# Kernel optimization log

Measured on AMD Instinct MI355X. Metric: run time of the kernel, lower is better.

Reference implementation:

```python
import jax, jax.numpy as jnp
import numpy as np

B = 8192      # graphs per batch
NPG = 40      # nodes per graph (= average_nodes, uniform here)
DEG = 16      # avg degree
IN = 64
HID = 32
OUT = 10
K1 = 20       # ceil(0.5*40)
K2 = 10       # ceil(0.5*20)
N = B * NPG
E = N * DEG
EPS = 1e-15


def _lin_params(k, fi, fo):
    kw, kb = jax.random.split(k)
    s = 1.0 / np.sqrt(fi)
    w = jax.random.uniform(kw, (fi, fo), jnp.float32, -s, s)
    b = jax.random.uniform(kb, (fo,), jnp.float32, -s, s)
    return w, b


def setup_inputs():
    key = jax.random.key(0)
    ks = jax.random.split(key, 14)
    x = jax.random.normal(ks[0], (N, IN), jnp.float32)
    # edges constrained within each graph (graphs are contiguous blocks of NPG nodes)
    g = jnp.repeat(jnp.arange(B, dtype=jnp.int32), NPG * DEG)
    src = g * NPG + jax.random.randint(ks[1], (E,), 0, NPG, dtype=jnp.int32)
    dst = g * NPG + jax.random.randint(ks[2], (E,), 0, NPG, dtype=jnp.int32)
    edge_index = jnp.stack([src, dst])
    batch = jnp.repeat(jnp.arange(B, dtype=jnp.int32), NPG)
    w_c1, b_c1 = _lin_params(ks[3], IN, HID)
    w_p1, b_p1 = _lin_params(ks[4], HID, K1)
    w2r, b2 = _lin_params(ks[5], HID, HID)
    w2o, _ = _lin_params(ks[6], HID, HID)
    w_p2, b_p2 = _lin_params(ks[7], HID, K2)
    w3r, b3 = _lin_params(ks[8], HID, HID)
    w3o, _ = _lin_params(ks[9], HID, HID)
    w_l1, b_l1 = _lin_params(ks[10], HID, HID)
    w_l2, b_l2 = _lin_params(ks[11], HID, OUT)
    return dict(x=x, edge_index=edge_index, batch=batch,
                w_c1=w_c1, b_c1=b_c1, w_p1=w_p1, b_p1=b_p1,
                w2r=w2r, b2=b2, w2o=w2o, w_p2=w_p2, b_p2=b_p2,
                w3r=w3r, b3=b3, w3o=w3o,
                w_l1=w_l1, b_l1=b_l1, w_l2=w_l2, b_l2=b_l2)


def _gcn_conv(x, edge_index, w, b):
    # PyG GCNConv: x' = D^-1/2 (A + I) D^-1/2 (X W) + b, unit edge weights
    h = x @ w
    row, col = edge_index
    deg = jnp.zeros((N,), h.dtype).at[col].add(1.0) + 1.0  # +1 self loop
    dinv = jax.lax.rsqrt(deg)
    msg = (dinv[row] * dinv[col])[:, None] * h[row]
    out = jnp.zeros_like(h).at[col].add(msg)
    out = out + (dinv * dinv)[:, None] * h  # self-loop contribution
    return out + b


def _dense_mincut_pool(x, adj, s, mask=None):
    # faithful to torch_geometric.nn.dense_mincut_pool
    s = jax.nn.softmax(s, axis=-1)
    if mask is not None:
        m = mask[..., None].astype(x.dtype)
        x = x * m
        s = s * m
    k = s.shape[-1]
    out = jnp.einsum('bnk,bnf->bkf', s, x)
    out_adj = jnp.einsum('bnk,bnm,bml->bkl', s, adj, s)
    mincut_num = jnp.trace(out_adj, axis1=1, axis2=2)
    d_flat = adj.sum(-1)                                   # [B, n]
    mincut_den = jnp.einsum('bnk,bn,bnk->b', s, d_flat, s)  # tr(S^T D S)
    mincut_loss = jnp.mean(-(mincut_num / mincut_den))
    ss = jnp.einsum('bnk,bnl->bkl', s, s)
    ss_norm = jnp.sqrt(jnp.sum(ss * ss, axis=(1, 2), keepdims=True))
    i_s = jnp.eye(k, dtype=x.dtype) / jnp.sqrt(jnp.asarray(k, x.dtype))
    ortho_loss = jnp.mean(jnp.sqrt(jnp.sum((ss / ss_norm - i_s) ** 2, axis=(1, 2))))
    # zero diagonal, then symmetric degree-normalize coarse adjacency
    eye = jnp.eye(k, dtype=x.dtype)
    out_adj = out_adj * (1.0 - eye)
    d = jnp.sqrt(out_adj.sum(-1))[:, None, :] + EPS        # [B,1,k]
    out_adj = out_adj / d / jnp.swapaxes(d, 1, 2)
    return out, out_adj, mincut_loss, ortho_loss


def _dense_graph_conv(x, adj, w_rel, b, w_root):
    # PyG DenseGraphConv (aggr='add'): lin_rel(A @ x) + lin_root(x); lin_root bias=False
    return (adj @ x) @ w_rel + b + x @ w_root


def reference(x, edge_index, batch, w_c1, b_c1, w_p1, b_p1, w2r, b2, w2o,
              w_p2, b_p2, w3r, b3, w3o, w_l1, b_l1, w_l2, b_l2):
    h = jax.nn.relu(_gcn_conv(x, edge_index, w_c1, b_c1))
    # to_dense_batch (uniform NPG nodes per graph, batch sorted)
    local = jnp.arange(N, dtype=jnp.int32) - batch * NPG
    xd = jnp.zeros((B, NPG, HID), h.dtype).at[batch, local].set(h)
    mask = jnp.ones((B, NPG), bool)
    # to_dense_adj (accumulates duplicate edges)
    row, col = edge_index
    g = batch[row]
    adj = jnp.zeros((B, NPG, NPG), h.dtype).at[g, row - g * NPG, col - g * NPG].add(1.0)
    s = xd @ w_p1 + b_p1
    xd, adj, mc1, o1 = _dense_mincut_pool(xd, adj, s, mask)
    xd = jax.nn.relu(_dense_graph_conv(xd, adj, w2r, b2, w2o))
    s = xd @ w_p2 + b_p2
    xd, adj, mc2, o2 = _dense_mincut_pool(xd, adj, s)
    xd = _dense_graph_conv(xd, adj, w3r, b3, w3o)
    pooled = xd.mean(axis=1)
    out = jax.nn.relu(pooled @ w_l1 + b_l1) @ w_l2 + b_l2
    return out, mc1 + mc2 + o1 + o2
```

## Files before the change

### kernel.cpp

```cpp
#include <hip/hip_runtime.h>

#define NT 256

constexpr int Bg   = 8192;
constexpr int NPG  = 40;
constexpr int EPG  = 640;
constexpr int IN_  = 64;
constexpr int HID  = 32;
constexpr int K1   = 20;
constexpr int K2   = 10;
constexpr int OUTC = 10;
constexpr int NE   = Bg * NPG * 16;
constexpr int SX   = 68;
constexpr int SH   = 36;
constexpr float EPSF = 1e-15f;

#define FMA4(acc, a, b) do { \
    float _s = (a); \
    acc.x = fmaf(_s, (b).x, acc.x); \
    acc.y = fmaf(_s, (b).y, acc.y); \
    acc.z = fmaf(_s, (b).z, acc.z); \
    acc.w = fmaf(_s, (b).w, acc.w); } while (0)

__device__ __forceinline__ float wave_red(float v) {
#pragma unroll
    for (int off = 32; off > 0; off >>= 1) v += __shfl_down(v, off, 64);
    return v;
}

__global__ __launch_bounds__(NT, 4)
void mincut_fused(const float* __restrict__ x, const int* __restrict__ ei,
                  const float* __restrict__ w_c1, const float* __restrict__ b_c1,
                  const float* __restrict__ w_p1, const float* __restrict__ b_p1,
                  const float* __restrict__ w2r_, const float* __restrict__ b2_,
                  const float* __restrict__ w2o_,
                  const float* __restrict__ w_p2, const float* __restrict__ b_p2,
                  const float* __restrict__ w3r_, const float* __restrict__ b3_,
                  const float* __restrict__ w3o_,
                  const float* __restrict__ w_l1, const float* __restrict__ b_l1,
                  const float* __restrict__ w_l2, const float* __restrict__ b_l2,
                  float* __restrict__ out, float* __restrict__ wsg)
{
    __shared__ __align__(16) float sA[NPG * NPG];
    __shared__ __align__(16) float sXbuf[NPG * SX];
    __shared__ __align__(16) float sH[NPG * SH];
    __shared__ __align__(16) float sXd[NPG * SH];
    __shared__ __align__(16) float sdinv[NPG];
    __shared__ __align__(16) float srowsA[NPG];
    __shared__ __align__(16) float srowm[NPG];
    __shared__ __align__(16) float sden[NPG];
    __shared__ __align__(16) float sc[8];

    float* sA2  = sA;
    float* sS   = sXbuf;
    float* sAS  = sXbuf + 800;
    float* sSS  = sXbuf + 1600;
    float* sX2  = sH;
    float* sS2  = sH + 720;
    float* sX3  = sH + 920;
    float* sA3  = sH + 1280;
    float* sXw2o= sXd;
    float* sW3r = sXd;
    float* sW3o = sXd + 360;
    float* sX4  = sH;

    const int g    = blockIdx.x;
    const int tid  = threadIdx.x;
    const int lane = tid & 63;
    const int wid  = tid >> 6;

    int er0, ec0, er1, ec1, er2 = -1, ec2 = 0;
    {
        const int eb = g * EPG, nb = g * NPG;
        int e = eb + tid;
        er0 = ei[e] - nb; ec0 = ei[NE + e] - nb;
        e += NT;
        er1 = ei[e] - nb; ec1 = ei[NE + e] - nb;
        if (tid + 2 * NT < EPG) {
            e += NT;
            er2 = ei[e] - nb; ec2 = ei[NE + e] - nb;
        }
    }
    for (int i = tid; i < NPG * NPG; i += NT) sA[i] = 0.f;
    {
        const float4* xg = (const float4*)(x + (size_t)g * (NPG * IN_));
        for (int i = tid; i < NPG * (IN_ / 4); i += NT) {
            int n = i >> 4, k = i & 15;
            ((float4*)(sXbuf + n * SX))[k] = xg[i];
        }
    }
    __syncthreads();

    atomicAdd(&sA[er0 * NPG + ec0], 1.f);
    atomicAdd(&sA[er1 * NPG + ec1], 1.f);
    if (er2 >= 0) atomicAdd(&sA[er2 * NPG + ec2], 1.f);

    if (tid < 160) {
        int np = tid >> 3, fq = tid & 7;
        int n0 = 2 * np, n1 = n0 + 1;
        const float4* a0p = (const float4*)(sXbuf + n0 * SX);
        const float4* a1p = (const float4*)(sXbuf + n1 * SX);
        const float4* wg  = (const float4*)w_c1;
        float4 acc0 = {0.f,0.f,0.f,0.f}, acc1 = {0.f,0.f,0.f,0.f};
#pragma unroll 4
        for (int kk = 0; kk < IN_ / 4; kk++) {
            float4 a0 = a0p[kk], a1 = a1p[kk];
            float4 w0 = wg[(4*kk+0)*8 + fq];
            float4 w1 = wg[(4*kk+1)*8 + fq];
            float4 w2 = wg[(4*kk+2)*8 + fq];
            float4 w3 = wg[(4*kk+3)*8 + fq];
            FMA4(acc0, a0.x, w0); FMA4(acc0, a0.y, w1);
            FMA4(acc0, a0.z, w2); FMA4(acc0, a0.w, w3);
            FMA4(acc1, a1.x, w0); FMA4(acc1, a1.y, w1);
            FMA4(acc1, a1.z, w2); FMA4(acc1, a1.w, w3);
        }
        ((float4*)(sH + n0 * SH))[fq] = acc0;
        ((float4*)(sH + n1 * SH))[fq] = acc1;
    }
    __syncthreads();

    if (tid < NPG) {
        float s = 0.f;
#pragma unroll
        for (int r = 0; r < NPG; r++) s += sA[r * NPG + tid];
        sdinv[tid] = rsqrtf(s + 1.f);
    } else if (tid >= 64 && tid < 64 + NPG) {
        int n = tid - 64; float s = 0.f;
#pragma unroll
        for (int m = 0; m < NPG; m++) s += sA[n * NPG + m];
        srowsA[n] = s;
    }
    __syncthreads();

    if (tid < 160) {
        int cp = tid >> 3, fq = tid & 7;
        int c0 = 2 * cp, c1 = c0 + 1;
        float4 acc0 = {0.f,0.f,0.f,0.f}, acc1 = {0.f,0.f,0.f,0.f};
#pragma unroll 8
        for (int r = 0; r < NPG; r++) {
            float2 a2 = *(const float2*)&sA[r * NPG + c0];
            float dv = sdinv[r];
            float4 bv = ((const float4*)(sH + r * SH))[fq];
            FMA4(acc0, a2.x * dv, bv);
            FMA4(acc1, a2.y * dv, bv);
        }
        float4 bb = ((const float4*)b_c1)[fq];
        float4 h0 = ((const float4*)(sH + c0 * SH))[fq];
        float4 h1 = ((const float4*)(sH + c1 * SH))[fq];
        float d0 = sdinv[c0], d1 = sdinv[c1];
        float4 r0, r1;
        r0.x = fmaxf(fmaf(d0, fmaf(d0, h0.x, acc0.x), bb.x), 0.f);
        r0.y = fmaxf(fmaf(d0, fmaf(d0, h0.y, acc0.y), bb.y), 0.f);
        r0.z = fmaxf(fmaf(d0, fmaf(d0, h0.z, acc0.z), bb.z), 0.f);
        r0.w = fmaxf(fmaf(d0, fmaf(d0, h0.w, acc0.w), bb.w), 0.f);
        r1.x = fmaxf(fmaf(d1, fmaf(d1, h1.x, acc1.x), bb.x), 0.f);
        r1.y = fmaxf(fmaf(d1, fmaf(d1, h1.y, acc1.y), bb.y), 0.f);
        r1.z = fmaxf(fmaf(d1, fmaf(d1, h1.z, acc1.z), bb.z), 0.f);
        r1.w = fmaxf(fmaf(d1, fmaf(d1, h1.w, acc1.w), bb.w), 0.f);
        ((float4*)(sXd + c0 * SH))[fq] = r0;
        ((float4*)(sXd + c1 * SH))[fq] = r1;
    }
    __syncthreads();

    if (tid < 100) {
        int np = tid / 5, lq = tid - np * 5;
        int n0 = 2 * np, n1 = n0 + 1;
        const float4* wg = (const float4*)w_p1;
        float4 bb = ((const float4*)b_p1)[lq];
        float4 acc0 = bb, acc1 = bb;
#pragma unroll 8
        for (int k = 0; k < HID; k++) {
            float a0 = sXd[n0 * SH + k];
            float a1 = sXd[n1 * SH + k];
            float4 w = wg[k * 5 + lq];
            FMA4(acc0, a0, w); FMA4(acc1, a1, w);
        }
        ((float4*)(sS + n0 * K1))[lq] = acc0;
        ((float4*)(sS + n1 * K1))[lq] = acc1;
    }
    __syncthreads();

    if (tid < NPG) {
        float* row = sS + tid * K1;
        float v[K1]; float m = -3.0e38f;
#pragma unroll
        for (int k = 0; k < K1; k++) { v[k] = row[k]; m = fmaxf(m, v[k]); }
        float ssum = 0.f;
#pragma unroll
        for (int k = 0; k < K1; k++) { v[k] = __expf(v[k] - m); ssum += v[k]; }
        float inv = 1.f / ssum;
#pragma unroll
        for (int k = 0; k < K1; k++) row[k] = v[k] * inv;
    }
    __syncthreads();

    if (tid < 100) {
        int np = tid / 5, lq = tid - np * 5;
        int n0 = 2 * np, n1 = n0 + 1;
        const float4* sb = (const float4*)sS;
        float4 acc0 = {0.f,0.f,0.f,0.f}, acc1 = {0.f,0.f,0.f,0.f};
#pragma unroll
        for (int m4 = 0; m4 < NPG / 4; m4++) {
            float4 a0 = *(const float4*)&sA[n0 * NPG + 4 * m4];
            float4 a1 = *(const float4*)&sA[n1 * NPG + 4 * m4];
            float4 b0 = sb[(4*m4+0)*5 + lq];
            float4 b1 = sb[(4*m4+1)*5 + lq];
            float4 b2v = sb[(4*m4+2)*5 + lq];
            float4 b3v = sb[(4*m4+3)*5 + lq];
            FMA4(acc0, a0.x, b0); FMA4(acc0, a0.y, b1);
            FMA4(acc0, a0.z, b2v); FMA4(acc0, a0.w, b3v);
            FMA4(acc1, a1.x, b0); FMA4(acc1, a1.y, b1);
            FMA4(acc1, a1.z, b2v); FMA4(acc1, a1.w, b3v);
        }
        ((float4*)(sAS + n0 * K1))[lq] = acc0;
        ((float4*)(sAS + n1 * K1))[lq] = acc1;
    } else if (tid < 150) {
        int oo = tid - 100;
        int kp = oo / 5, lq = oo - kp * 5;
        int k0 = 2 * kp, k1 = k0 + 1;
        float4 acc0 = {0.f,0.f,0.f,0.f}, acc1 = {0.f,0.f,0.f,0.f};
#pragma unroll 8
        for (int n = 0; n < NPG; n++) {
            float2 s2v = *(const float2*)&sS[n * K1 + k0];
            float4 bv = ((const float4*)(sS + n * K1))[lq];
            FMA4(acc0, s2v.x, bv); FMA4(acc1, s2v.y, bv);
        }
        ((float4*)(sSS + k0 * K1))[lq] = acc0;
        ((float4*)(sSS + k1 * K1))[lq] = acc1;
    }
    __syncthreads();

    if (tid < 50) {
        int kp = tid / 5, lq = tid - kp * 5;
        int k0 = 2 * kp, k1 = k0 + 1;
        float4 acc0 = {0.f,0.f,0.f,0.f}, acc1 = {0.f,0.f,0.f,0.f};
#pragma unroll 8
        for (int n = 0; n < NPG; n++) {
            float2 s2v = *(const float2*)&sS[n * K1 + k0];
            float4 bv = ((const float4*)(sAS + n * K1))[lq];
            FMA4(acc0, s2v.x, bv); FMA4(acc1, s2v.y, bv);
        }
        ((float4*)(sA2 + k0 * K1))[lq] = acc0;
        ((float4*)(sA2 + k1 * K1))[lq] = acc1;
    } else if (tid < 130) {
        int oo = tid - 50;
        int kp = oo >> 3, fq = oo & 7;
        int k0 = 2 * kp, k1 = k0 + 1;
        float4 acc0 = {0.f,0.f,0.f,0.f}, acc1 = {0.f,0.f,0.f,0.f};
#pragma unroll 8
        for (int n = 0; n < NPG; n++) {
            float2 s2v = *(const float2*)&sS[n * K1 + k0];
            float4 bv = ((const float4*)(sXd + n * SH))[fq];
            FMA4(acc0, s2v.x, bv); FMA4(acc1, s2v.y, bv);
        }
        ((float4*)(sX2 + k0 * SH))[fq] = acc0;
        ((float4*)(sX2 + k1 * SH))[fq] = acc1;
    } else if (tid < 170) {
        int n = tid - 130;
        float s2 = 0.f;
#pragma unroll
        for (int k = 0; k < K1; k++) { float v = sS[n * K1 + k]; s2 = fmaf(v, v, s2); }
        sden[n] = srowsA[n] * s2;
    }
    __syncthreads();

    if (wid == 0) {
        float f = 0.f, tr = 0.f;
        for (int i = lane; i < K1 * K1; i += 64) {
            float t = sSS[i];
            f = fmaf(t, t, f);
            if (i % (K1 + 1) == 0) tr += t;
        }
        f = wave_red(f); tr = wave_red(tr);
        if (lane == 0)
            sc[2] = sqrtf(fmaxf(2.f - 2.f * tr / (sqrtf(f) * 4.47213595499958f), 0.f));
    } else if (wid == 1) {
        float v = 0.f;
        if (lane < K1) {
            float s = 0.f;
#pragma unroll
            for (int l = 0; l < K1; l++) s += sA2[lane * K1 + l];
            float d = sA2[lane * (K1 + 1)];
            srowm[lane] = 1.f / (sqrtf(s - d) + EPSF);
            v = d;
        }
        v = wave_red(v);
        if (lane == 0) sc[0] = v;
    } else if (wid == 2) {
        float v = (lane < NPG) ? sden[lane] : 0.f;
        v = wave_red(v);
        if (lane == 0) sc[1] = v;
    }
    if (tid < 160) {
        int n = tid >> 3, fq = tid & 7;
        const float4* wg = (const float4*)w2o_;
        float4 acc = {0.f,0.f,0.f,0.f};
#pragma unroll 8
        for (int k = 0; k < HID; k++) {
            float a = sX2[n * SH + k];
            FMA4(acc, a, wg[k * 8 + fq]);
        }
        ((float4*)(sXw2o + n * SH))[fq] = acc;
    }
    __syncthreads();

    if (tid < 160) {
        int k = tid >> 3, fq = tid & 7;
        float4 acc = {0.f,0.f,0.f,0.f};
#pragma unroll
        for (int l = 0; l < K1; l++) {
            float a = (l == k) ? 0.f : sA2[k * K1 + l];
            float4 bv = ((const float4*)(sX2 + l * SH))[fq];
            FMA4(acc, a * srowm[l], bv);
        }
        float rk = srowm[k];
        acc.x *= rk; acc.y *= rk; acc.z *= rk; acc.w *= rk;
        ((float4*)(sAS + k * SH))[fq] = acc;
    }
    __syncthreads();

    if (tid < 160) {
        int k = tid >> 3, fq = tid & 7;
        const float4* wg = (const float4*)w2r_;
        float4 bb = ((const float4*)b2_)[fq];
        float4 oo = ((const float4*)(sXw2o + k * SH))[fq];
        float4 acc;
        acc.x = bb.x + oo.x; acc.y = bb.y + oo.y;
        acc.z = bb.z + oo.z; acc.w = bb.w + oo.w;
#pragma unroll 8
        for (int j = 0; j < HID; j++) {
            float a = sAS[k * SH + j];
            FMA4(acc, a, wg[j * 8 + fq]);
        }
        acc.x = fmaxf(acc.x, 0.f); acc.y = fmaxf(acc.y, 0.f);
        acc.z = fmaxf(acc.z, 0.f); acc.w = fmaxf(acc.w, 0.f);
        ((float4*)(sX2 + k * SH))[fq] = acc;
    }
    __syncthreads();

    if (tid < K1 * K2) {
        int n = tid / K2, q = tid - n * K2;
        float acc = b_p2[q];
#pragma unroll 8
        for (int j = 0; j < HID; j++) acc = fmaf(sX2[n * SH + j], w_p2[j * K2 + q], acc);
        sS2[tid] = acc;
    }
    __syncthreads();

    if (tid < K1) {
        float* row = sS2 + tid * K2;
        float v[K2]; float m = -3.0e38f;
#pragma unroll
        for (int q = 0; q < K2; q++) { v[q] = row[q]; m = fmaxf(m, v[q]); }
        float ssum = 0.f;
#pragma unroll
        for (int q = 0; q < K2; q++) { v[q] = __expf(v[q] - m); ssum += v[q]; }
        float inv = 1.f / ssum;
#pragma unroll
        for (int q = 0; q < K2; q++) row[q] = v[q] * inv;
    }
    __syncthreads();

    for (int o = tid; o < 400; o += NT) {
        if (o < 200) {
            int n = o / K2, l = o - n * K2;
            float acc = 0.f;
#pragma unroll
            for (int m = 0; m < K1; m++) {
                float a = (m == n) ? 0.f : sA2[n * K1 + m];
                acc = fmaf(a * srowm[m], sS2[m * K2 + l], acc);
            }
            sAS[n * K2 + l] = acc * srowm[n];
        } else if (o < 300) {
            int oo = o - 200; int k = oo / K2, l = oo - k * K2;
            float acc = 0.f;
#pragma unroll
            for (int n = 0; n < K1; n++) acc = fmaf(sS2[n * K2 + k], sS2[n * K2 + l], acc);
            sSS[oo] = acc;
        } else if (o < 380) {
            int oo = o - 300; int k = oo >> 3, fq = oo & 7;
            float4 acc = {0.f,0.f,0.f,0.f};
#pragma unroll
            for (int n = 0; n < K1; n++) {
                float a = sS2[n * K2 + k];
                float4 bv = ((const float4*)(sX2 + n * SH))[fq];
                FMA4(acc, a, bv);
            }
            ((float4*)(sX3 + k * SH))[fq] = acc;
        } else {
            int n = o - 380;
            float da = 0.f, s2 = 0.f;
#pragma unroll
            for (int l = 0; l < K1; l++) {
                float a = (l == n) ? 0.f : sA2[n * K1 + l];
                da = fmaf(a, srowm[l], da);
            }
            da *= srowm[n];
#pragma unroll
            for (int q = 0; q < K2; q++) { float v = sS2[n * K2 + q]; s2 = fmaf(v, v, s2); }
            sden[n] = da * s2;
        }
    }
    __syncthreads();

    if (tid < K2 * K2) {
        int k = tid / K2, l = tid - k * K2;
        float acc = 0.f;
#pragma unroll
        for (int n = 0; n < K1; n++) acc = fmaf(sS2[n * K2 + k], sAS[n * K2 + l], acc);
        sA3[tid] = acc;
    } else if (wid == 2) {
        float v = (lane < K1) ? sden[lane] : 0.f;
        v = wave_red(v);
        if (lane == 0) sc[5] = v;
    } else if (wid == 3) {
        float f = 0.f, tr = 0.f;
        for (int i = lane; i < K2 * K2; i += 64) {
            float t = sSS[i];
            f = fmaf(t, t, f);
            if (i % (K2 + 1) == 0) tr += t;
        }
        f = wave_red(f); tr = wave_red(tr);
        if (lane == 0)
            sc[6] = sqrtf(fmaxf(2.f - 2.f * tr / (sqrtf(f) * 3.1622776601683795f), 0.f));
    }
    __syncthreads();

    if (tid < 160) {
        bool first = (tid < 80);
        int oo = first ? tid : tid - 80;
        int n = oo >> 3, fq = oo & 7;
        const float4* wg = (const float4*)(first ? w3r_ : w3o_);
        float4 acc = {0.f,0.f,0.f,0.f};
#pragma unroll 8
        for (int k = 0; k < HID; k++) {
            float a = sX3[n * SH + k];
            FMA4(acc, a, wg[k * 8 + fq]);
        }
        if (first) ((float4*)(sW3r + n * SH))[fq] = acc;
        else       ((float4*)(sW3o + n * SH))[fq] = acc;
    } else if (tid >= 160 && tid < 160 + K2) {
        int l = tid - 160;
        float s = 0.f;
#pragma unroll
        for (int m = 0; m < K2; m++) s += sA3[l * K2 + m];
        s -= sA3[l * (K2 + 1)];
        srowm[l] = 1.f / (sqrtf(s) + EPSF);
    } else if (tid == 200) {
        float num2 = 0.f;
#pragma unroll
        for (int k = 0; k < K2; k++) num2 += sA3[k * (K2 + 1)];
        wsg[g] = -(sc[0] / sc[1]) + sc[2] - num2 / sc[5] + sc[6];
    }
    __syncthreads();

    if (tid < 80) {
        int k = tid >> 3, fq = tid & 7;
        float4 acc = {0.f,0.f,0.f,0.f};
#pragma unroll
        for (int l = 0; l < K2; l++) {
            float a = (l == k) ? 0.f : sA3[k * K2 + l];
            float4 w = ((const float4*)(sW3r + l * SH))[fq];
            FMA4(acc, a * srowm[l], w);
        }
        float4 bb = ((const float4*)b3_)[fq];
        float4 oo = ((const float4*)(sW3o + k * SH))[fq];
        float rk = srowm[k];
        float4 r;
        r.x = fmaf(rk, acc.x, oo.x + bb.x);
        r.y = fmaf(rk, acc.y, oo.y + bb.y);
        r.z = fmaf(rk, acc.z, oo.z + bb.z);
        r.w = fmaf(rk, acc.w, oo.w + bb.w);
        ((float4*)(sX4 + k * SH))[fq] = r;
    }
    __syncthreads();

    if (wid == 0) {
        int f = lane & 31;
        float pool = 0.f;
#pragma unroll
        for (int n = 0; n < K2; n++) pool += sX4[n * SH + f];
        pool *= (1.f / K2);
        float acc = b_l1[f];
#pragma unroll
        for (int j = 0; j < HID; j++)
            acc = fmaf(__shfl(pool, j, 64), w_l1[j * HID + f], acc);
        float t1 = fmaxf(acc, 0.f);
        int o = (lane < OUTC) ? lane : 0;
        float acc2 = b_l2[o];
#pragma unroll
        for (int j = 0; j < HID; j++)
            acc2 = fmaf(__shfl(t1, j, 64), w_l2[j * OUTC + o], acc2);
        if (lane < OUTC) out[(size_t)g * OUTC + lane] = acc2;
    }
}

__global__ void loss_reduce(const float* __restrict__ wsg, float* __restrict__ out)
{
    __shared__ float sred[4];
    int tid = threadIdx.x;
    float s = 0.f;
    for (int i = tid; i < Bg; i += NT) s += wsg[i];
    s = wave_red(s);
    if ((tid & 63) == 0) sred[tid >> 6] = s;
    __syncthreads();
    if (tid == 0) out[(size_t)Bg * OUTC] = (sred[0] + sred[1] + sred[2] + sred[3]) * (1.f / Bg);
}

extern "C" void kernel_launch(void* const* d_in, const int* in_sizes, int n_in,
                              void* d_out, int out_size, void* d_ws, size_t ws_size,
                              hipStream_t stream)
{
    const float* x    = (const float*)d_in[0];
    const int*   ei   = (const int*)  d_in[1];
    const float* w_c1 = (const float*)d_in[3];
    const float* b_c1 = (const float*)d_in[4];
    const float* w_p1 = (const float*)d_in[5];
    const float* b_p1 = (const float*)d_in[6];
    const float* w2r  = (const float*)d_in[7];
    const float* b2   = (const float*)d_in[8];
    const float* w2o  = (const float*)d_in[9];
    const float* w_p2 = (const float*)d_in[10];
    const float* b_p2 = (const float*)d_in[11];
    const float* w3r  = (const float*)d_in[12];
    const float* b3   = (const float*)d_in[13];
    const float* w3o  = (const float*)d_in[14];
    const float* w_l1 = (const float*)d_in[15];
    const float* b_l1 = (const float*)d_in[16];
    const float* w_l2 = (const float*)d_in[17];
    const float* b_l2 = (const float*)d_in[18];
    float* out = (float*)d_out;
    float* wsg = (float*)d_ws;

    hipLaunchKernelGGL(mincut_fused, dim3(Bg), dim3(NT), 0, stream,
                       x, ei, w_c1, b_c1, w_p1, b_p1, w2r, b2, w2o,
                       w_p2, b_p2, w3r, b3, w3o, w_l1, b_l1, w_l2, b_l2,
                       out, wsg);
    hipLaunchKernelGGL(loss_reduce, dim3(1), dim3(NT), 0, stream, wsg, out);
}
```

Before: 258.3 us.

## Merge shared buffers and fuse stage-2 conv and pool-score stages to cut syncs

Merges the x-buffer and h-buffer into one aliased shared array so LDS per block shrinks, which could allow more resident blocks per CU. To make that aliasing safe, GCN linear results are kept in registers across a barrier before being stored, and the degree/row-sum pass is merged into the same phase. The stage-2 graph conv is reassociated so both weight products are computed first, then the adjacency aggregation, bias, and relu happen in one pass. The pool-2 score projection is fused with its softmax. Together these remove several barriers, at the cost of more register pressure and more intricate buffer reuse.

```diff
diff --git a/kernel.cpp b/kernel.cpp
--- a/kernel.cpp
+++ b/kernel.cpp
@@ -42,8 +42,7 @@
                   float* __restrict__ out, float* __restrict__ wsg)
 {
     __shared__ __align__(16) float sA[NPG * NPG];
-    __shared__ __align__(16) float sXbuf[NPG * SX];
-    __shared__ __align__(16) float sH[NPG * SH];
+    __shared__ __align__(16) float sB[NPG * SX];
     __shared__ __align__(16) float sXd[NPG * SH];
     __shared__ __align__(16) float sdinv[NPG];
     __shared__ __align__(16) float srowsA[NPG];
@@ -52,17 +51,20 @@
     __shared__ __align__(16) float sc[8];
 
     float* sA2  = sA;
-    float* sS   = sXbuf;
-    float* sAS  = sXbuf + 800;
-    float* sSS  = sXbuf + 1600;
-    float* sX2  = sH;
-    float* sS2  = sH + 720;
-    float* sX3  = sH + 920;
-    float* sA3  = sH + 1280;
-    float* sXw2o= sXd;
+    float* sA3  = sA + 400;
+    float* sH   = sB;
+    float* sS   = sB;
+    float* sAS  = sB + 800;
+    float* sS2  = sB + 800;
+    float* sAS2 = sB + 1000;
+    float* sX3  = sB + 1200;
+    float* sX4  = sB + 1200;
+    float* sSS  = sB + 1600;
+    float* sX2  = sB + 2000;
+    float* sXw2r= sXd;
+    float* sXw2o= sXd + 720;
     float* sW3r = sXd;
     float* sW3o = sXd + 360;
-    float* sX4  = sH;
 
     const int g    = blockIdx.x;
     const int tid  = threadIdx.x;
@@ -86,7 +88,7 @@
         const float4* xg = (const float4*)(x + (size_t)g * (NPG * IN_));
         for (int i = tid; i < NPG * (IN_ / 4); i += NT) {
             int n = i >> 4, k = i & 15;
-            ((float4*)(sXbuf + n * SX))[k] = xg[i];
+            ((float4*)(sB + n * SX))[k] = xg[i];
         }
     }
     __syncthreads();
@@ -95,13 +97,13 @@
     atomicAdd(&sA[er1 * NPG + ec1], 1.f);
     if (er2 >= 0) atomicAdd(&sA[er2 * NPG + ec2], 1.f);
 
+    float4 hacc0 = {0.f,0.f,0.f,0.f}, hacc1 = {0.f,0.f,0.f,0.f};
     if (tid < 160) {
         int np = tid >> 3, fq = tid & 7;
         int n0 = 2 * np, n1 = n0 + 1;
-        const float4* a0p = (const float4*)(sXbuf + n0 * SX);
-        const float4* a1p = (const float4*)(sXbuf + n1 * SX);
+        const float4* a0p = (const float4*)(sB + n0 * SX);
+        const float4* a1p = (const float4*)(sB + n1 * SX);
         const float4* wg  = (const float4*)w_c1;
-        float4 acc0 = {0.f,0.f,0.f,0.f}, acc1 = {0.f,0.f,0.f,0.f};
 #pragma unroll 4
         for (int kk = 0; kk < IN_ / 4; kk++) {
             float4 a0 = a0p[kk], a1 = a1p[kk];
@@ -109,23 +111,26 @@
             float4 w1 = wg[(4*kk+1)*8 + fq];
             float4 w2 = wg[(4*kk+2)*8 + fq];
             float4 w3 = wg[(4*kk+3)*8 + fq];
-            FMA4(acc0, a0.x, w0); FMA4(acc0, a0.y, w1);
-            FMA4(acc0, a0.z, w2); FMA4(acc0, a0.w, w3);
-            FMA4(acc1, a1.x, w0); FMA4(acc1, a1.y, w1);
-            FMA4(acc1, a1.z, w2); FMA4(acc1, a1.w, w3);
-        }
-        ((float4*)(sH + n0 * SH))[fq] = acc0;
-        ((float4*)(sH + n1 * SH))[fq] = acc1;
-    }
-    __syncthreads();
-
-    if (tid < NPG) {
-        float s = 0.f;
-#pragma unroll
-        for (int r = 0; r < NPG; r++) s += sA[r * NPG + tid];
-        sdinv[tid] = rsqrtf(s + 1.f);
-    } else if (tid >= 64 && tid < 64 + NPG) {
-        int n = tid - 64; float s = 0.f;
+            FMA4(hacc0, a0.x, w0); FMA4(hacc0, a0.y, w1);
+            FMA4(hacc0, a0.z, w2); FMA4(hacc0, a0.w, w3);
+            FMA4(hacc1, a1.x, w0); FMA4(hacc1, a1.y, w1);
+            FMA4(hacc1, a1.z, w2); FMA4(hacc1, a1.w, w3);
+        }
+    }
+    __syncthreads();
+
+    if (tid < 160) {
+        int np = tid >> 3, fq = tid & 7;
+        int n0 = 2 * np, n1 = n0 + 1;
+        ((float4*)(sH + n0 * SH))[fq] = hacc0;
+        ((float4*)(sH + n1 * SH))[fq] = hacc1;
+    } else if (tid < 200) {
+        int c = tid - 160; float s = 0.f;
+#pragma unroll
+        for (int r = 0; r < NPG; r++) s += sA[r * NPG + c];
+        sdinv[c] = rsqrtf(s + 1.f);
+    } else if (tid < 240) {
+        int n = tid - 200; float s = 0.f;
 #pragma unroll
         for (int m = 0; m < NPG; m++) s += sA[n * NPG + m];
         srowsA[n] = s;
@@ -197,16 +202,16 @@
     if (tid < 100) {
         int np = tid / 5, lq = tid - np * 5;
         int n0 = 2 * np, n1 = n0 + 1;
-        const float4* sb = (const float4*)sS;
+        const float4* sb4 = (const float4*)sS;
         float4 acc0 = {0.f,0.f,0.f,0.f}, acc1 = {0.f,0.f,0.f,0.f};
 #pragma unroll
         for (int m4 = 0; m4 < NPG / 4; m4++) {
             float4 a0 = *(const float4*)&sA[n0 * NPG + 4 * m4];
             float4 a1 = *(const float4*)&sA[n1 * NPG + 4 * m4];
-            float4 b0 = sb[(4*m4+0)*5 + lq];
-            float4 b1 = sb[(4*m4+1)*5 + lq];
-            float4 b2v = sb[(4*m4+2)*5 + lq];
-            float4 b3v = sb[(4*m4+3)*5 + lq];
+            float4 b0 = sb4[(4*m4+0)*5 + lq];
+            float4 b1 = sb4[(4*m4+1)*5 + lq];
+            float4 b2v = sb4[(4*m4+2)*5 + lq];
+            float4 b3v = sb4[(4*m4+3)*5 + lq];
             FMA4(acc0, a0.x, b0); FMA4(acc0, a0.y, b1);
             FMA4(acc0, a0.z, b2v); FMA4(acc0, a0.w, b3v);
             FMA4(acc1, a1.x, b0); FMA4(acc1, a1.y, b1);
@@ -291,16 +296,17 @@
         v = wave_red(v);
         if (lane == 0) sc[1] = v;
     }
-    if (tid < 160) {
-        int n = tid >> 3, fq = tid & 7;
-        const float4* wg = (const float4*)w2o_;
+    for (int o = tid; o < 320; o += NT) {
+        int first = o < 160; int m = first ? o : o - 160;
+        int n = m >> 3, fq = m & 7;
+        const float4* wg = (const float4*)(first ? w2r_ : w2o_);
         float4 acc = {0.f,0.f,0.f,0.f};
 #pragma unroll 8
         for (int k = 0; k < HID; k++) {
             float a = sX2[n * SH + k];
             FMA4(acc, a, wg[k * 8 + fq]);
         }
-        ((float4*)(sXw2o + n * SH))[fq] = acc;
+        ((float4*)((first ? sXw2r : sXw2o) + n * SH))[fq] = acc;
     }
     __syncthreads();
 
@@ -310,54 +316,40 @@
 #pragma unroll
         for (int l = 0; l < K1; l++) {
             float a = (l == k) ? 0.f : sA2[k * K1 + l];
-            float4 bv = ((const float4*)(sX2 + l * SH))[fq];
-            FMA4(acc, a * srowm[l], bv);
-        }
-        float rk = srowm[k];
-        acc.x *= rk; acc.y *= rk; acc.z *= rk; acc.w *= rk;
-        ((float4*)(sAS + k * SH))[fq] = acc;
-    }
-    __syncthreads();
-
-    if (tid < 160) {
-        int k = tid >> 3, fq = tid & 7;
-        const float4* wg = (const float4*)w2r_;
+            float4 w = ((const float4*)(sXw2r + l * SH))[fq];
+            FMA4(acc, a * srowm[l], w);
+        }
         float4 bb = ((const float4*)b2_)[fq];
         float4 oo = ((const float4*)(sXw2o + k * SH))[fq];
-        float4 acc;
-        acc.x = bb.x + oo.x; acc.y = bb.y + oo.y;
-        acc.z = bb.z + oo.z; acc.w = bb.w + oo.w;
+        float rk = srowm[k];
+        float4 r;
+        r.x = fmaxf(fmaf(rk, acc.x, oo.x + bb.x), 0.f);
+        r.y = fmaxf(fmaf(rk, acc.y, oo.y + bb.y), 0.f);
+        r.z = fmaxf(fmaf(rk, acc.z, oo.z + bb.z), 0.f);
+        r.w = fmaxf(fmaf(rk, acc.w, oo.w + bb.w), 0.f);
+        ((float4*)(sX2 + k * SH))[fq] = r;
+    }
+    __syncthreads();
+
+    if (tid < K1) {
+        float acc[K2];
+#pragma unroll
+        for (int q = 0; q < K2; q++) acc[q] = b_p2[q];
 #pragma unroll 8
         for (int j = 0; j < HID; j++) {
-            float a = sAS[k * SH + j];
-            FMA4(acc, a, wg[j * 8 + fq]);
-        }
-        acc.x = fmaxf(acc.x, 0.f); acc.y = fmaxf(acc.y, 0.f);
-        acc.z = fmaxf(acc.z, 0.f); acc.w = fmaxf(acc.w, 0.f);
-        ((float4*)(sX2 + k * SH))[fq] = acc;
-    }
-    __syncthreads();
-
-    if (tid < K1 * K2) {
-        int n = tid / K2, q = tid - n * K2;
-        float acc = b_p2[q];
-#pragma unroll 8
-        for (int j = 0; j < HID; j++) acc = fmaf(sX2[n * SH + j], w_p2[j * K2 + q], acc);
-        sS2[tid] = acc;
-    }
-    __syncthreads();
-
-    if (tid < K1) {
-        float* row = sS2 + tid * K2;
-        float v[K2]; float m = -3.0e38f;
-#pragma unroll
-        for (int q = 0; q < K2; q++) { v[q] = row[q]; m = fmaxf(m, v[q]); }
+            float a = sX2[tid * SH + j];
+#pragma unroll
+            for (int q = 0; q < K2; q++) acc[q] = fmaf(a, w_p2[j * K2 + q], acc[q]);
+        }
+        float m = -3.0e38f;
+#pragma unroll
+        for (int q = 0; q < K2; q++) m = fmaxf(m, acc[q]);
         float ssum = 0.f;
 #pragma unroll
-        for (int q = 0; q < K2; q++) { v[q] = __expf(v[q] - m); ssum += v[q]; }
+        for (int q = 0; q < K2; q++) { acc[q] = __expf(acc[q] - m); ssum += acc[q]; }
         float inv = 1.f / ssum;
 #pragma unroll
-        for (int q = 0; q < K2; q++) row[q] = v[q] * inv;
+        for (int q = 0; q < K2; q++) sS2[tid * K2 + q] = acc[q] * inv;
     }
     __syncthreads();
 
@@ -370,7 +362,7 @@
                 float a = (m == n) ? 0.f : sA2[n * K1 + m];
                 acc = fmaf(a * srowm[m], sS2[m * K2 + l], acc);
             }
-            sAS[n * K2 + l] = acc * srowm[n];
+            sAS2[n * K2 + l] = acc * srowm[n];
         } else if (o < 300) {
             int oo = o - 200; int k = oo / K2, l = oo - k * K2;
             float acc = 0.f;
@@ -407,7 +399,7 @@
         int k = tid / K2, l = tid - k * K2;
         float acc = 0.f;
 #pragma unroll
-        for (int n = 0; n < K1; n++) acc = fmaf(sS2[n * K2 + k], sAS[n * K2 + l], acc);
+        for (int n = 0; n < K1; n++) acc = fmaf(sS2[n * K2 + k], sAS2[n * K2 + l], acc);
         sA3[tid] = acc;
     } else if (wid == 2) {
         float v = (lane < K1) ? sden[lane] : 0.f;
```

New measurement: 246.5 us. -4.5%, faster.
